# Performance work log

Hardware: AMD Instinct MI355X
Metric: run time of the kernel (lower is better)

The kernel has to match this reference:

```python
import jax, jax.numpy as jnp
import numpy as np

BETA = 0.25

def setup_inputs() -> dict:
    key = jax.random.key(0)
    k1, k2 = jax.random.split(key)
    z = jax.random.normal(k1, (32, 256, 32, 32), dtype=jnp.float32)
    # embedding init ~ U(-1/K, 1/K) as intended by the module
    K, D = 1024, 256
    codebook = jax.random.uniform(k2, (K, D), dtype=jnp.float32, minval=-1.0 / K, maxval=1.0 / K)
    return {"z": z, "codebook": codebook}


def reference(z, codebook):
    # z: [B, D, H, W] -> [B, H, W, D]
    zt = jnp.transpose(z, (0, 2, 3, 1))
    B, H, W, D = zt.shape
    z_flat = zt.reshape(-1, D)  # [N, D]
    # pairwise squared distance: ||z||^2 + ||e||^2 - 2 z e^T
    dist = (
        jnp.sum(z_flat * z_flat, axis=1, keepdims=True)
        + jnp.sum(codebook * codebook, axis=1)[None, :]
        - 2.0 * jnp.matmul(z_flat, codebook.T)
    )  # [N, K]
    idx = jnp.argmin(dist, axis=1)  # [N]
    z_q = codebook[idx].reshape(B, H, W, D)
    sg = jax.lax.stop_gradient
    loss = jnp.mean((sg(z_q) - zt) ** 2) + BETA * jnp.mean((sg(zt) - z_q) ** 2)
    # straight-through estimator
    z_q = zt + sg(z_q - zt)
    z_q = jnp.transpose(z_q, (0, 3, 1, 2))  # back to [B, D, H, W]
    return z_q, idx, loss
```

## Files before the change

### kernel.cpp

```cpp
#include <hip/hip_runtime.h>
#include <stdint.h>


#define D_DIM   256
#define HW      1024
#define MT      64
#define THREADS 512
#define LIST_CAP 2048

#define ZQ_OFF   0
#define IDX_OFF  8388608
#define LOSS_OFF 8421376

typedef __attribute__((ext_vector_type(8))) short  short8;
typedef __attribute__((ext_vector_type(4))) float  f32x4;
typedef __attribute__((ext_vector_type(4))) unsigned int u32x4;

#define ZFP_ROW   264
#define OFF_ZFP   0
#define OFF_HEB   67584
#define OFF_LEB   83968
#define OFF_HZA   100352
#define OFF_LZA   104448
#define OFF_LIST  108544
#define OFF_ZN    116736
#define OFF_DLT   116992
#define OFF_RMIN  117248
#define OFF_RBV   117504
#define OFF_RBK   117760
#define OFF_BESTM 118016
#define OFF_CNT   118272
#define OFF_OVF   118276
#define SMEM_BYTES 118288

#define SWZ(rowi, u16) (((u16) ^ ((((rowi) >> 1) & 3) << 4)))

extern __shared__ char smc[];

__global__ void enorm_kernel(const float* __restrict__ cb, float* __restrict__ enorm) {
    int gt = blockIdx.x * blockDim.x + threadIdx.x;
    int k = gt >> 6;
    int lane = gt & 63;
    const float4* row = (const float4*)(cb + (size_t)k * D_DIM);
    float4 v = row[lane];
    float s = fmaf(v.x, v.x, fmaf(v.y, v.y, fmaf(v.z, v.z, v.w * v.w)));
    #pragma unroll
    for (int off = 32; off; off >>= 1) s += __shfl_xor(s, off);
    if (lane == 0) enorm[k] = s;
}

__device__ __forceinline__ void split2(float a, float b, unsigned &hi, unsigned &lo) {
    unsigned ba = __float_as_uint(a), bb = __float_as_uint(b);
    unsigned ha = ba & 0xFFFF0000u, hb = bb & 0xFFFF0000u;
    float ra = a - __uint_as_float(ha);
    float rb = b - __uint_as_float(hb);
    hi = (ha >> 16) | hb;
    lo = (__float_as_uint(ra) >> 16) | (__float_as_uint(rb) & 0xFFFF0000u);
}

__device__ __forceinline__ void split8(const float* src, u32x4 &hv, u32x4 &lv) {
    f32x4 A0 = *(const f32x4*)(src);
    f32x4 A1 = *(const f32x4*)(src + 4);
    unsigned h0, l0, h1, l1, h2, l2, h3, l3;
    split2(A0.x, A0.y, h0, l0);
    split2(A0.z, A0.w, h1, l1);
    split2(A1.x, A1.y, h2, l2);
    split2(A1.z, A1.w, h3, l3);
    hv.x = h0; hv.y = h1; hv.z = h2; hv.w = h3;
    lv.x = l0; lv.y = l1; lv.z = l2; lv.w = l3;
}

__device__ __noinline__ float exact_val(const char* sm, const float* cb,
                                        const float* enorm, int m, int k) {
    const float* zr = (const float*)(sm + OFF_ZFP) + (size_t)m * ZFP_ROW;
    const float* cr = cb + (size_t)k * D_DIM;
    float dot = 0.f;
    #pragma unroll 8
    for (int d = 0; d < D_DIM; ++d) dot = fmaf(zr[d], cr[d], dot);
    float A = ((const float*)(sm + OFF_ZN))[m] + enorm[k];
    return A - 2.0f * dot;
}

__global__ __launch_bounds__(THREADS, 2)
void vq_kernel(const float* __restrict__ z, const float* __restrict__ cb,
               const float* __restrict__ enorm, float* __restrict__ out)
{
    char* sm = smc;
    float*    zfp   = (float*)(sm + OFF_ZFP);
    float*    znS   = (float*)(sm + OFF_ZN);
    float*    dltS  = (float*)(sm + OFF_DLT);
    unsigned* rminU = (unsigned*)(sm + OFF_RMIN);
    unsigned* rbv   = (unsigned*)(sm + OFF_RBV);
    unsigned* rbk   = (unsigned*)(sm + OFF_RBK);
    int*      bestm = (int*)(sm + OFF_BESTM);
    unsigned* listU = (unsigned*)(sm + OFF_LIST);
    int*      cntP  = (int*)(sm + OFF_CNT);
    int*      ovfP  = (int*)(sm + OFF_OVF);

    const int t   = threadIdx.x;
    const int blk = blockIdx.x;
    const int b   = blk >> 4;
    const int p0  = (blk & 15) * MT;
    const float* zb = z + (size_t)b * D_DIM * HW;

    #pragma unroll
    for (int r = 0; r < 8; ++r) {
        int d = (t >> 4) + r * 32;
        int m4 = (t & 15) * 4;
        f32x4 v = *(const f32x4*)(zb + (size_t)d * HW + p0 + m4);
        zfp[(m4 + 0) * ZFP_ROW + d] = v.x;
        zfp[(m4 + 1) * ZFP_ROW + d] = v.y;
        zfp[(m4 + 2) * ZFP_ROW + d] = v.z;
        zfp[(m4 + 3) * ZFP_ROW + d] = v.w;
    }
    __syncthreads();

    {
        int m = t & 63, q = t >> 6;
        const float* zr = zfp + m * ZFP_ROW + q * 32;
        double zp = 0.0;
        #pragma unroll 8
        for (int d = 0; d < 32; ++d) { double v = (double)zr[d]; zp += v * v; }
        double* zscr = (double*)(sm + OFF_HEB);
        zscr[q * 64 + m] = zp;
    }
    __syncthreads();
    if (t < 64) {
        double* zscr = (double*)(sm + OFF_HEB);
        double s = 0.0;
        #pragma unroll
        for (int q = 0; q < 8; ++q) s += zscr[q * 64 + t];
        float zn = (float)s;
        znS[t]  = zn;
        dltS[t] = 1.15e-5f * sqrtf(zn) + 9.5e-5f;
        rbv[t]  = 0x7f800000u;
        rbk[t]  = 0xFFFFFFFFu;
    }
    if (t == 0) { *cntP = 0; *ovfP = 0; }
    __syncthreads();

    const int l   = t & 63;
    const int wid = t >> 6;
    const int wm  = wid & 3;
    const int wc  = wid >> 2;
    const int l15 = l & 15;

    for (int kc = 0; kc < 4; ++kc) {
        if (t < 64) rminU[t] = 0x7f800000u;

        f32x4 acc[8];
        #pragma unroll
        for (int sc = 0; sc < 8; ++sc) acc[sc] = (f32x4){0.f, 0.f, 0.f, 0.f};

        for (int s = 0; s < 8; ++s) {
            const int d0 = s * 32;
            __syncthreads();

            #pragma unroll
            for (int i = 0; i < 2; ++i) {
                int id = i * 512 + t;
                int u = id & 3, code = id >> 2;
                const float* src = cb + (size_t)(kc * 256 + code) * D_DIM + d0 + u * 8;
                u32x4 hv, lv;
                split8(src, hv, lv);
                int off = code * 64 + SWZ(code, u * 16);
                *(u32x4*)(sm + OFF_HEB + off) = hv;
                *(u32x4*)(sm + OFF_LEB + off) = lv;
            }
            {
                int m = (t >> 2) & 63, u = t & 3, arr = t >> 8;
                const float* zr = zfp + m * ZFP_ROW + d0 + u * 8;
                u32x4 hv, lv;
                split8(zr, hv, lv);
                int off = m * 64 + SWZ(m, u * 16);
                *(u32x4*)(sm + (arr ? OFF_LZA : OFF_HZA) + off) = arr ? lv : hv;
            }
            __syncthreads();

            int arow = wm * 16 + l15;
            int aoff = arow * 64 + SWZ(arow, (l >> 4) * 16);
            short8 hzF = *(const short8*)(sm + OFF_HZA + aoff);
            short8 lzF = *(const short8*)(sm + OFF_LZA + aoff);
            #pragma unroll
            for (int c4 = 0; c4 < 2; ++c4) {
                short8 he[4], le[4];
                #pragma unroll
                for (int j = 0; j < 4; ++j) {
                    int codeL = wc * 128 + (c4 * 4 + j) * 16 + l15;
                    int boff = codeL * 64 + SWZ(codeL, (l >> 4) * 16);
                    he[j] = *(const short8*)(sm + OFF_HEB + boff);
                    le[j] = *(const short8*)(sm + OFF_LEB + boff);
                }
                #pragma unroll
                for (int j = 0; j < 4; ++j)
                    acc[c4*4+j] = __builtin_amdgcn_mfma_f32_16x16x32_bf16(hzF, he[j], acc[c4*4+j], 0, 0, 0);
                #pragma unroll
                for (int j = 0; j < 4; ++j)
                    acc[c4*4+j] = __builtin_amdgcn_mfma_f32_16x16x32_bf16(hzF, le[j], acc[c4*4+j], 0, 0, 0);
                #pragma unroll
                for (int j = 0; j < 4; ++j)
                    acc[c4*4+j] = __builtin_amdgcn_mfma_f32_16x16x32_bf16(lzF, he[j], acc[c4*4+j], 0, 0, 0);
            }
        }

        float bn[8];
        #pragma unroll
        for (int sc = 0; sc < 8; ++sc)
            bn[sc] = enorm[kc * 256 + wc * 128 + sc * 16 + l15];

        #pragma unroll
        for (int reg = 0; reg < 4; ++reg) {
            int row = wm * 16 + (l >> 4) * 4 + reg;
            float zn = znS[row];
            float vmin = 3.4e38f;
            #pragma unroll
            for (int sc = 0; sc < 8; ++sc) {
                float val = (zn + bn[sc]) - 2.0f * acc[sc][reg];
                vmin = fminf(vmin, val);
            }
            #pragma unroll
            for (int off = 8; off; off >>= 1) vmin = fminf(vmin, __shfl_xor(vmin, off));
            if (l15 == 0) atomicMin(&rminU[row], __float_as_uint(vmin));
        }
        __syncthreads();

        #pragma unroll
        for (int reg = 0; reg < 4; ++reg) {
            int row = wm * 16 + (l >> 4) * 4 + reg;
            float thr = __uint_as_float(rminU[row]) + dltS[row];
            float zn = znS[row];
            #pragma unroll
            for (int sc = 0; sc < 8; ++sc) {
                float val = (zn + bn[sc]) - 2.0f * acc[sc][reg];
                if (val <= thr) {
                    int slot = atomicAdd(cntP, 1);
                    int kg = kc * 256 + wc * 128 + sc * 16 + l15;
                    if (slot < LIST_CAP) listU[slot] = ((unsigned)row << 16) | (unsigned)kg;
                    else *ovfP = 1;
                }
            }
        }
        __syncthreads();
    }

    const int n = min(*cntP, LIST_CAP);
    const int isovf = *ovfP;
    if (!isovf) {
        for (int i = t; i < n; i += THREADS) {
            unsigned e = listU[i];
            float val = exact_val(sm, cb, enorm, (int)(e >> 16), (int)(e & 0xFFFFu));
            atomicMin(&rbv[e >> 16], __float_as_uint(val));
        }
        __syncthreads();
        for (int i = t; i < n; i += THREADS) {
            unsigned e = listU[i];
            int m = (int)(e >> 16), k = (int)(e & 0xFFFFu);
            float val = exact_val(sm, cb, enorm, m, k);
            if (__float_as_uint(val) == rbv[m]) atomicMin(&rbk[m], (unsigned)k);
        }
    } else {
        for (int id = t; id < MT * 1024; id += THREADS) {
            float val = exact_val(sm, cb, enorm, id >> 10, id & 1023);
            atomicMin(&rbv[id >> 10], __float_as_uint(val));
        }
        __syncthreads();
        for (int id = t; id < MT * 1024; id += THREADS) {
            int m = id >> 10, k = id & 1023;
            float val = exact_val(sm, cb, enorm, m, k);
            if (__float_as_uint(val) == rbv[m]) atomicMin(&rbk[m], (unsigned)k);
        }
    }
    __syncthreads();

    if (t < 64) {
        int k = (int)rbk[t];
        bestm[t] = k;
        out[IDX_OFF + (size_t)blk * MT + t] = (float)k;
    }
    __syncthreads();

    float lsum = 0.f;
    const size_t zq_base = (size_t)b * D_DIM * HW + p0;
    for (int i2 = t; i2 < D_DIM * MT / 4; i2 += THREADS) {
        int p = i2 & (MT - 1), d4 = i2 >> 6;
        int idx = bestm[p];
        f32x4 cv = *(const f32x4*)(cb + (size_t)idx * D_DIM + d4 * 4);
        const float* zr = zfp + p * ZFP_ROW + d4 * 4;
        float z0 = zr[0], z1 = zr[1], z2 = zr[2], z3 = zr[3];
        float e0 = cv.x - z0, e1 = cv.y - z1, e2 = cv.z - z2, e3 = cv.w - z3;
        lsum = fmaf(e0, e0, lsum); lsum = fmaf(e1, e1, lsum);
        lsum = fmaf(e2, e2, lsum); lsum = fmaf(e3, e3, lsum);
        out[zq_base + (size_t)(d4 * 4 + 0) * HW + p] = cv.x;
        out[zq_base + (size_t)(d4 * 4 + 1) * HW + p] = cv.y;
        out[zq_base + (size_t)(d4 * 4 + 2) * HW + p] = cv.z;
        out[zq_base + (size_t)(d4 * 4 + 3) * HW + p] = cv.w;
    }
    #pragma unroll
    for (int off = 32; off; off >>= 1) lsum += __shfl_xor(lsum, off);
    __syncthreads();
    float* lscr = (float*)(sm + OFF_LIST);
    if ((t & 63) == 0) lscr[t >> 6] = lsum;
    __syncthreads();
    if (t == 0) {
        float s = 0.f;
        #pragma unroll
        for (int w = 0; w < 8; ++w) s += lscr[w];
        atomicAdd(out + LOSS_OFF, s * (1.25f / 8388608.f));
    }
}

extern "C" void kernel_launch(void* const* d_in, const int* in_sizes, int n_in,
                              void* d_out, int out_size, void* d_ws, size_t ws_size,
                              hipStream_t stream) {
    const float* z  = (const float*)d_in[0];
    const float* cb = (const float*)d_in[1];
    float* out = (float*)d_out;
    float* enorm = (float*)d_ws;

    hipMemsetAsync(out + LOSS_OFF, 0, sizeof(float), stream);

    enorm_kernel<<<256, 256, 0, stream>>>(cb, enorm);

    hipFuncSetAttribute((const void*)vq_kernel,
                        hipFuncAttributeMaxDynamicSharedMemorySize, SMEM_BYTES);
    vq_kernel<<<512, THREADS, SMEM_BYTES, stream>>>(z, cb, enorm, out);
}
```

Measured before the change: 273.5 us.

## Presplit codebook into bf16 hi/lo workspace and keep z fragments in registers

Adds a split_kernel that converts the codebook once per call into pre-swizzled bf16 hi/lo tiles in workspace, so the main kernel only copies them into LDS instead of re-splitting on every tile. The z tile is no longer staged in LDS. Each wave loads its A fragments for all depth steps straight from global memory into registers, and the exact-distance and loss passes read z from global memory. This cuts LDS from about 118KB to 42KB, which may allow more blocks per CU, at the cost of more registers, strided global reads of z, and an extra kernel launch.

```diff
diff --git a/kernel.cpp b/kernel.cpp
--- a/kernel.cpp
+++ b/kernel.cpp
@@ -16,24 +16,24 @@
 typedef __attribute__((ext_vector_type(4))) float  f32x4;
 typedef __attribute__((ext_vector_type(4))) unsigned int u32x4;
 
-#define ZFP_ROW   264
-#define OFF_ZFP   0
-#define OFF_HEB   67584
-#define OFF_LEB   83968
-#define OFF_HZA   100352
-#define OFF_LZA   104448
-#define OFF_LIST  108544
-#define OFF_ZN    116736
-#define OFF_DLT   116992
-#define OFF_RMIN  117248
-#define OFF_RBV   117504
-#define OFF_RBK   117760
-#define OFF_BESTM 118016
-#define OFF_CNT   118272
-#define OFF_OVF   118276
-#define SMEM_BYTES 118288
+#define OFF_HEB   0
+#define OFF_LEB   16384
+#define OFF_LIST  32768
+#define OFF_ZN    40960
+#define OFF_DLT   41216
+#define OFF_RMIN  41472
+#define OFF_RBV   41728
+#define OFF_RBK   41984
+#define OFF_BESTM 42240
+#define OFF_CNT   42496
+#define OFF_OVF   42500
+#define SMEM_BYTES 42512
 
 #define SWZ(rowi, u16) (((u16) ^ ((((rowi) >> 1) & 3) << 4)))
+
+#define WS_B_OFF   4096
+#define WS_B_BYTES 1048576
+#define WS_NEEDED  (WS_B_OFF + WS_B_BYTES)
 
 extern __shared__ char smc[];
 
@@ -70,23 +70,36 @@
     lv.x = l0; lv.y = l1; lv.z = l2; lv.w = l3;
 }
 
-__device__ __noinline__ float exact_val(const char* sm, const float* cb,
-                                        const float* enorm, int m, int k) {
-    const float* zr = (const float*)(sm + OFF_ZFP) + (size_t)m * ZFP_ROW;
+__global__ void split_kernel(const float* __restrict__ cb, char* __restrict__ wsB) {
+    int id = blockIdx.x * blockDim.x + threadIdx.x;
+    int g = id >> 10, rem = id & 1023, code = rem >> 2, slot = rem & 3;
+    int kc = g >> 3, s = g & 7;
+    int u = slot ^ ((code >> 1) & 3);
+    const float* src = cb + (size_t)(kc * 256 + code) * D_DIM + s * 32 + u * 8;
+    u32x4 hv, lv;
+    split8(src, hv, lv);
+    char* dst = wsB + (size_t)g * 32768 + (size_t)(code * 4 + slot) * 16;
+    *(u32x4*)dst = hv;
+    *(u32x4*)(dst + 16384) = lv;
+}
+
+__device__ __noinline__ float exact_val(const float* zcol, const float* cb,
+                                        const float* enorm, const float* znArr,
+                                        int m, int k) {
     const float* cr = cb + (size_t)k * D_DIM;
     float dot = 0.f;
     #pragma unroll 8
-    for (int d = 0; d < D_DIM; ++d) dot = fmaf(zr[d], cr[d], dot);
-    float A = ((const float*)(sm + OFF_ZN))[m] + enorm[k];
-    return A - 2.0f * dot;
-}
-
+    for (int d = 0; d < D_DIM; ++d) dot = fmaf(zcol[(size_t)d * HW + m], cr[d], dot);
+    return (znArr[m] + enorm[k]) - 2.0f * dot;
+}
+
+template <int PRESPLIT>
 __global__ __launch_bounds__(THREADS, 2)
 void vq_kernel(const float* __restrict__ z, const float* __restrict__ cb,
-               const float* __restrict__ enorm, float* __restrict__ out)
+               const float* __restrict__ enorm, const char* __restrict__ wsB,
+               float* __restrict__ out)
 {
     char* sm = smc;
-    float*    zfp   = (float*)(sm + OFF_ZFP);
     float*    znS   = (float*)(sm + OFF_ZN);
     float*    dltS  = (float*)(sm + OFF_DLT);
     unsigned* rminU = (unsigned*)(sm + OFF_RMIN);
@@ -101,26 +114,18 @@
     const int blk = blockIdx.x;
     const int b   = blk >> 4;
     const int p0  = (blk & 15) * MT;
-    const float* zb = z + (size_t)b * D_DIM * HW;
-
-    #pragma unroll
-    for (int r = 0; r < 8; ++r) {
-        int d = (t >> 4) + r * 32;
-        int m4 = (t & 15) * 4;
-        f32x4 v = *(const f32x4*)(zb + (size_t)d * HW + p0 + m4);
-        zfp[(m4 + 0) * ZFP_ROW + d] = v.x;
-        zfp[(m4 + 1) * ZFP_ROW + d] = v.y;
-        zfp[(m4 + 2) * ZFP_ROW + d] = v.z;
-        zfp[(m4 + 3) * ZFP_ROW + d] = v.w;
-    }
-    __syncthreads();
+    const float* zb   = z + (size_t)b * D_DIM * HW;
+    const float* zcol = zb + p0;
 
     {
         int m = t & 63, q = t >> 6;
-        const float* zr = zfp + m * ZFP_ROW + q * 32;
+        const float* col = zcol + m;
         double zp = 0.0;
         #pragma unroll 8
-        for (int d = 0; d < 32; ++d) { double v = (double)zr[d]; zp += v * v; }
+        for (int d = q * 32; d < q * 32 + 32; ++d) {
+            double v = (double)col[(size_t)d * HW];
+            zp += v * v;
+        }
         double* zscr = (double*)(sm + OFF_HEB);
         zscr[q * 64 + m] = zp;
     }
@@ -137,13 +142,40 @@
         rbk[t]  = 0xFFFFFFFFu;
     }
     if (t == 0) { *cntP = 0; *ovfP = 0; }
-    __syncthreads();
 
     const int l   = t & 63;
     const int wid = t >> 6;
     const int wm  = wid & 3;
     const int wc  = wid >> 2;
     const int l15 = l & 15;
+    const int hi4 = l >> 4;
+
+    short8 AH[8], AL[8];
+    {
+        const float* zA = zcol + wm * 16 + l15;
+        #pragma unroll
+        for (int s = 0; s < 8; ++s) {
+            const float* ap = zA + (size_t)(s * 32 + hi4 * 8) * HW;
+            float v0 = ap[0];
+            float v1 = ap[(size_t)1 * HW];
+            float v2 = ap[(size_t)2 * HW];
+            float v3 = ap[(size_t)3 * HW];
+            float v4 = ap[(size_t)4 * HW];
+            float v5 = ap[(size_t)5 * HW];
+            float v6 = ap[(size_t)6 * HW];
+            float v7 = ap[(size_t)7 * HW];
+            unsigned h0, l0, h1, l1, h2, l2, h3, l3;
+            split2(v0, v1, h0, l0);
+            split2(v2, v3, h1, l1);
+            split2(v4, v5, h2, l2);
+            split2(v6, v7, h3, l3);
+            u32x4 hv; hv.x = h0; hv.y = h1; hv.z = h2; hv.w = h3;
+            u32x4 lv; lv.x = l0; lv.y = l1; lv.z = l2; lv.w = l3;
+            AH[s] = __builtin_bit_cast(short8, hv);
+            AL[s] = __builtin_bit_cast(short8, lv);
+        }
+    }
+    __syncthreads();
 
     for (int kc = 0; kc < 4; ++kc) {
         if (t < 64) rminU[t] = 0x7f800000u;
@@ -152,42 +184,43 @@
         #pragma unroll
         for (int sc = 0; sc < 8; ++sc) acc[sc] = (f32x4){0.f, 0.f, 0.f, 0.f};
 
+        #pragma unroll
         for (int s = 0; s < 8; ++s) {
-            const int d0 = s * 32;
             __syncthreads();
-
-            #pragma unroll
-            for (int i = 0; i < 2; ++i) {
-                int id = i * 512 + t;
-                int u = id & 3, code = id >> 2;
-                const float* src = cb + (size_t)(kc * 256 + code) * D_DIM + d0 + u * 8;
-                u32x4 hv, lv;
-                split8(src, hv, lv);
-                int off = code * 64 + SWZ(code, u * 16);
-                *(u32x4*)(sm + OFF_HEB + off) = hv;
-                *(u32x4*)(sm + OFF_LEB + off) = lv;
-            }
-            {
-                int m = (t >> 2) & 63, u = t & 3, arr = t >> 8;
-                const float* zr = zfp + m * ZFP_ROW + d0 + u * 8;
-                u32x4 hv, lv;
-                split8(zr, hv, lv);
-                int off = m * 64 + SWZ(m, u * 16);
-                *(u32x4*)(sm + (arr ? OFF_LZA : OFF_HZA) + off) = arr ? lv : hv;
+            if (PRESPLIT) {
+                const char* src = wsB + (size_t)(kc * 8 + s) * 32768;
+                #pragma unroll
+                for (int i = 0; i < 2; ++i) {
+                    int id = i * 512 + t;
+                    u32x4 hv = *(const u32x4*)(src + (size_t)id * 16);
+                    u32x4 lv = *(const u32x4*)(src + 16384 + (size_t)id * 16);
+                    *(u32x4*)(sm + OFF_HEB + id * 16) = hv;
+                    *(u32x4*)(sm + OFF_LEB + id * 16) = lv;
+                }
+            } else {
+                #pragma unroll
+                for (int i = 0; i < 2; ++i) {
+                    int id = i * 512 + t;
+                    int u = id & 3, code = id >> 2;
+                    const float* srcf = cb + (size_t)(kc * 256 + code) * D_DIM + s * 32 + u * 8;
+                    u32x4 hv, lv;
+                    split8(srcf, hv, lv);
+                    int off = code * 64 + SWZ(code, u * 16);
+                    *(u32x4*)(sm + OFF_HEB + off) = hv;
+                    *(u32x4*)(sm + OFF_LEB + off) = lv;
+                }
             }
             __syncthreads();
 
-            int arow = wm * 16 + l15;
-            int aoff = arow * 64 + SWZ(arow, (l >> 4) * 16);
-            short8 hzF = *(const short8*)(sm + OFF_HZA + aoff);
-            short8 lzF = *(const short8*)(sm + OFF_LZA + aoff);
+            const short8 hzF = AH[s];
+            const short8 lzF = AL[s];
             #pragma unroll
             for (int c4 = 0; c4 < 2; ++c4) {
                 short8 he[4], le[4];
                 #pragma unroll
                 for (int j = 0; j < 4; ++j) {
                     int codeL = wc * 128 + (c4 * 4 + j) * 16 + l15;
-                    int boff = codeL * 64 + SWZ(codeL, (l >> 4) * 16);
+                    int boff = codeL * 64 + SWZ(codeL, hi4 * 16);
                     he[j] = *(const short8*)(sm + OFF_HEB + boff);
                     le[j] = *(const short8*)(sm + OFF_LEB + boff);
                 }
@@ -210,7 +243,7 @@
 
         #pragma unroll
         for (int reg = 0; reg < 4; ++reg) {
-            int row = wm * 16 + (l >> 4) * 4 + reg;
+            int row = wm * 16 + hi4 * 4 + reg;
             float zn = znS[row];
             float vmin = 3.4e38f;
             #pragma unroll
@@ -226,7 +259,7 @@
 
         #pragma unroll
         for (int reg = 0; reg < 4; ++reg) {
-            int row = wm * 16 + (l >> 4) * 4 + reg;
+            int row = wm * 16 + hi4 * 4 + reg;
             float thr = __uint_as_float(rminU[row]) + dltS[row];
             float zn = znS[row];
             #pragma unroll
@@ -248,25 +281,25 @@
     if (!isovf) {
         for (int i = t; i < n; i += THREADS) {
             unsigned e = listU[i];
-            float val = exact_val(sm, cb, enorm, (int)(e >> 16), (int)(e & 0xFFFFu));
+            float val = exact_val(zcol, cb, enorm, znS, (int)(e >> 16), (int)(e & 0xFFFFu));
             atomicMin(&rbv[e >> 16], __float_as_uint(val));
         }
         __syncthreads();
         for (int i = t; i < n; i += THREADS) {
             unsigned e = listU[i];
             int m = (int)(e >> 16), k = (int)(e & 0xFFFFu);
-            float val = exact_val(sm, cb, enorm, m, k);
+            float val = exact_val(zcol, cb, enorm, znS, m, k);
             if (__float_as_uint(val) == rbv[m]) atomicMin(&rbk[m], (unsigned)k);
         }
     } else {
         for (int id = t; id < MT * 1024; id += THREADS) {
-            float val = exact_val(sm, cb, enorm, id >> 10, id & 1023);
+            float val = exact_val(zcol, cb, enorm, znS, id >> 10, id & 1023);
             atomicMin(&rbv[id >> 10], __float_as_uint(val));
         }
         __syncthreads();
         for (int id = t; id < MT * 1024; id += THREADS) {
             int m = id >> 10, k = id & 1023;
-            float val = exact_val(sm, cb, enorm, m, k);
+            float val = exact_val(zcol, cb, enorm, znS, m, k);
             if (__float_as_uint(val) == rbv[m]) atomicMin(&rbk[m], (unsigned)k);
         }
     }
@@ -285,8 +318,11 @@
         int p = i2 & (MT - 1), d4 = i2 >> 6;
         int idx = bestm[p];
         f32x4 cv = *(const f32x4*)(cb + (size_t)idx * D_DIM + d4 * 4);
-        const float* zr = zfp + p * ZFP_ROW + d4 * 4;
-        float z0 = zr[0], z1 = zr[1], z2 = zr[2], z3 = zr[3];
+        const float* zp = zcol + p;
+        float z0 = zp[(size_t)(d4 * 4 + 0) * HW];
+        float z1 = zp[(size_t)(d4 * 4 + 1) * HW];
+        float z2 = zp[(size_t)(d4 * 4 + 2) * HW];
+        float z3 = zp[(size_t)(d4 * 4 + 3) * HW];
         float e0 = cv.x - z0, e1 = cv.y - z1, e2 = cv.z - z2, e3 = cv.w - z3;
         lsum = fmaf(e0, e0, lsum); lsum = fmaf(e1, e1, lsum);
         lsum = fmaf(e2, e2, lsum); lsum = fmaf(e3, e3, lsum);
@@ -316,12 +352,20 @@
     const float* cb = (const float*)d_in[1];
     float* out = (float*)d_out;
     float* enorm = (float*)d_ws;
+    char*  wsB   = (char*)d_ws + WS_B_OFF;
 
     hipMemsetAsync(out + LOSS_OFF, 0, sizeof(float), stream);
 
     enorm_kernel<<<256, 256, 0, stream>>>(cb, enorm);
 
-    hipFuncSetAttribute((const void*)vq_kernel,
-                        hipFuncAttributeMaxDynamicSharedMemorySize, SMEM_BYTES);
-    vq_kernel<<<512, THREADS, SMEM_BYTES, stream>>>(z, cb, enorm, out);
-}
+    if (ws_size >= (size_t)WS_NEEDED) {
+        split_kernel<<<128, 256, 0, stream>>>(cb, wsB);
+        hipFuncSetAttribute((const void*)vq_kernel<1>,
+                            hipFuncAttributeMaxDynamicSharedMemorySize, SMEM_BYTES);
+        vq_kernel<1><<<512, THREADS, SMEM_BYTES, stream>>>(z, cb, enorm, wsB, out);
+    } else {
+        hipFuncSetAttribute((const void*)vq_kernel<0>,
+                            hipFuncAttributeMaxDynamicSharedMemorySize, SMEM_BYTES);
+        vq_kernel<0><<<512, THREADS, SMEM_BYTES, stream>>>(z, cb, enorm, wsB, out);
+    }
+}
```

Measured after the change: 252.9 us. 7.5% less time.
